# Kernel tuning notes

Measured on AMD Instinct MI355X. Metric: run time of the kernel, lower is better.

The kernel has to match this reference:

```python
import jax, jax.numpy as jnp
import numpy as np

HS = 2048   # hidden_size
NH = 16     # num_attention_heads
HD = HS // NH  # head_dim = 128
FD = 256    # feature_dim
EPS = 1e-5  # layer_norm_epsilon


def setup_inputs() -> dict:
    key = jax.random.key(0)
    ks = jax.random.split(key, 12)
    s = 0.02
    return {
        "hidden_states": jax.random.normal(ks[0], (2, 4096, HS), jnp.float32),
        "attention_mask": jnp.zeros((2, 4096), jnp.float32),
        "Wq": jax.random.normal(ks[1], (HS, HS), jnp.float32) * s,
        "bq": jnp.zeros((HS,), jnp.float32),
        "Wk": jax.random.normal(ks[2], (HS, HS), jnp.float32) * s,
        "bk": jnp.zeros((HS,), jnp.float32),
        "Wv": jax.random.normal(ks[3], (HS, HS), jnp.float32) * s,
        "bv": jnp.zeros((HS,), jnp.float32),
        "Wo": jax.random.normal(ks[4], (HS, HS), jnp.float32) * s,
        "bo": jnp.zeros((HS,), jnp.float32),
        "Wf1": jax.random.normal(ks[5], (HD, FD), jnp.float32) * s,
        "bf1": jnp.zeros((FD,), jnp.float32),
        "Wf2": jax.random.normal(ks[6], (FD, FD), jnp.float32) * s,
        "bf2": jnp.zeros((FD,), jnp.float32),
        "ln_g": jnp.ones((FD,), jnp.float32),
        "ln_b": jnp.zeros((FD,), jnp.float32),
    }


def reference(hidden_states, attention_mask, Wq, bq, Wk, bk, Wv, bv, Wo, bo,
              Wf1, bf1, Wf2, bf2, ln_g, ln_b):
    B, L, H = hidden_states.shape

    # QKV projections -> [B, NH, L, HD]
    q = (hidden_states @ Wq + bq).reshape(B, L, NH, HD).transpose(0, 2, 1, 3)
    k = (hidden_states @ Wk + bk).reshape(B, L, NH, HD).transpose(0, 2, 1, 3)
    v = (hidden_states @ Wv + bv).reshape(B, L, NH, HD).transpose(0, 2, 1, 3)

    # seq_len (4096) > linear_threshold (1024) -> linear attention branch
    def feature_map(x):  # Linear -> ReLU -> Linear -> LayerNorm
        h = jax.nn.relu(x @ Wf1 + bf1)
        h = h @ Wf2 + bf2
        mu = jnp.mean(h, axis=-1, keepdims=True)
        var = jnp.var(h, axis=-1, keepdims=True)  # biased, like torch LayerNorm
        return (h - mu) * jax.lax.rsqrt(var + EPS) * ln_g + ln_b

    q_feat = feature_map(q)  # [B, NH, L, FD]
    k_feat = feature_map(k)
    # attention_mask [B, L] -> k_feat * (1 + mask)
    k_feat = k_feat * (1.0 + attention_mask[:, None, :, None])

    kv = jnp.einsum('bhlf,bhld->bhfd', k_feat, v)          # [B, NH, FD, HD]
    attn = jnp.einsum('bhlf,bhfd->bhld', q_feat, kv)       # [B, NH, L, HD]
    k_sum = jnp.sum(k_feat, axis=2)                         # [B, NH, FD]
    denom = jnp.einsum('bhlf,bhf->bhl', q_feat, k_sum)[..., None]
    attn = attn / (denom + 1e-8)

    attn = attn.transpose(0, 2, 1, 3).reshape(B, L, H)
    return attn @ Wo + bo
```

## Files before the change

kernel.cpp:

```cpp
#include <hip/hip_runtime.h>

typedef unsigned short u16;
typedef unsigned int u32;
typedef __attribute__((ext_vector_type(8))) short bf16x8;
typedef __attribute__((ext_vector_type(4))) float f32x4;

#define B_ 2
#define L_ 4096
#define HS_ 2048
#define NH_ 16
#define HD_ 128
#define FD_ 256

__device__ __forceinline__ float bf2f(u16 u) { return __uint_as_float(((u32)u) << 16); }
__device__ __forceinline__ u16 f2bf(float f) {
    u32 x = __float_as_uint(f);
    return (u16)((x + 0x7fffu + ((x >> 16) & 1u)) >> 16);
}

__device__ __forceinline__ void llds16(const u16* g, u16* l) {
    __builtin_amdgcn_global_load_lds((const __attribute__((address_space(1))) void*)g,
                                     (__attribute__((address_space(3))) void*)l, 16, 0, 0);
}

__device__ __forceinline__ void gemm_mainloop(const u16* __restrict__ Ab, int lda,
                                              const u16* __restrict__ Bb, int ldb,
                                              int K, u16* As, u16* Bs, f32x4 (&acc)[4][4]) {
    const int tid  = threadIdx.x;
    const int lane = tid & 63;
    const int wave = tid >> 6;
    const int wm = wave >> 1, wn = wave & 1;

    f32x4 zero = {0.f, 0.f, 0.f, 0.f};
#pragma unroll
    for (int i = 0; i < 4; i++)
#pragma unroll
        for (int j = 0; j < 4; j++) acc[i][j] = zero;

    const int srow = lane >> 2;
    const int scol = (lane & 3) * 8;
    const u16* pa = Ab + (size_t)(wave * 32 + srow) * lda + scol;
    const u16* pb = Bb + (size_t)(wave * 32 + srow) * ldb + scol;
    u16* la = As + wave * 1024;
    u16* lb = Bs + wave * 1024;

    const int arow = (wm * 64 + (lane & 15)) * 32 + (lane >> 4) * 8;
    const int brow = (wn * 64 + (lane & 15)) * 32 + (lane >> 4) * 8;

    for (int k0 = 0; k0 < K; k0 += 32) {
        llds16(pa, la);
        llds16(pa + 16 * lda, la + 512);
        llds16(pb, lb);
        llds16(pb + 16 * ldb, lb + 512);
        pa += 32; pb += 32;
        __syncthreads();
        bf16x8 af[4], bg[4];
#pragma unroll
        for (int mt = 0; mt < 4; mt++) af[mt] = *(const bf16x8*)(As + arow + mt * 512);
#pragma unroll
        for (int nt = 0; nt < 4; nt++) bg[nt] = *(const bf16x8*)(Bs + brow + nt * 512);
#pragma unroll
        for (int mt = 0; mt < 4; mt++)
#pragma unroll
            for (int nt = 0; nt < 4; nt++)
                acc[mt][nt] = __builtin_amdgcn_mfma_f32_16x16x32_bf16(af[mt], bg[nt], acc[mt][nt], 0, 0, 0);
        __syncthreads();
    }
}

__global__ __launch_bounds__(256) void k_cvt(const float* __restrict__ src, u16* __restrict__ dst) {
    size_t i = ((size_t)blockIdx.x * 256 + threadIdx.x) * 8;
    float4 a = *(const float4*)(src + i);
    float4 b = *(const float4*)(src + i + 4);
    union { u16 h[8]; uint4 v; } o;
    o.h[0] = f2bf(a.x); o.h[1] = f2bf(a.y); o.h[2] = f2bf(a.z); o.h[3] = f2bf(a.w);
    o.h[4] = f2bf(b.x); o.h[5] = f2bf(b.y); o.h[6] = f2bf(b.z); o.h[7] = f2bf(b.w);
    *(uint4*)(dst + i) = o.v;
}

__global__ __launch_bounds__(256) void k_transpose(const float* Wq, const float* Wk, const float* Wv,
                                                   const float* Wo, const float* Wf1, const float* Wf2,
                                                   u16* Wqkv_t, u16* Wo_t, u16* Wf1_t, u16* Wf2_t) {
    const float* src; u16* dst; int R, C;
    switch (blockIdx.z) {
        case 0: src = Wq;  dst = Wqkv_t;                R = 2048; C = 2048; break;
        case 1: src = Wk;  dst = Wqkv_t + 2048 * 2048;  R = 2048; C = 2048; break;
        case 2: src = Wv;  dst = Wqkv_t + 2 * 2048 * 2048; R = 2048; C = 2048; break;
        case 3: src = Wo;  dst = Wo_t;                  R = 2048; C = 2048; break;
        case 4: src = Wf1; dst = Wf1_t;                 R = 128;  C = 256;  break;
        default: src = Wf2; dst = Wf2_t;                R = 256;  C = 256;  break;
    }
    int c0 = blockIdx.x * 32, r0 = blockIdx.y * 32;
    if (c0 >= C || r0 >= R) return;
    __shared__ u16 tile[32][33];
    int tx = threadIdx.x, ty = threadIdx.y;
    for (int i = ty; i < 32; i += 8) tile[i][tx] = f2bf(src[(size_t)(r0 + i) * C + c0 + tx]);
    __syncthreads();
    for (int i = ty; i < 32; i += 8) dst[(size_t)(c0 + i) * R + r0 + tx] = tile[tx][i];
}

#define QKV_BAR() { __builtin_amdgcn_sched_barrier(0); __builtin_amdgcn_s_barrier(); \
                    __builtin_amdgcn_sched_barrier(0); }
#define QKV_LGKM0() { asm volatile("s_waitcnt lgkmcnt(0)" ::: "memory"); \
                      __builtin_amdgcn_sched_barrier(0); }

__device__ __forceinline__ void mainloop256(const u16* __restrict__ Abase,
                                            const u16* __restrict__ Bbase,
                                            u16* LDS, f32x4 (&acc)[8][4]) {
    const int tid = threadIdx.x, lane = tid & 63, wave = tid >> 6;
    const int wm = wave >> 2, wn = wave & 3;

    int r0g, c0g, r1g, c1g;
    { int p = tid * 16; int s = p >> 10, q = p & 1023; q ^= ((q >> 9) & 1) << 5;
      r0g = (s >> 1) * 16 + (q >> 6); c0g = (s & 1) * 32 + ((q & 63) >> 1); }
    { int p = 8192 + tid * 16; int s = p >> 10, q = p & 1023; q ^= ((q >> 9) & 1) << 5;
      r1g = (s >> 1) * 16 + (q >> 6); c1g = (s & 1) * 32 + ((q & 63) >> 1); }
    const int voff0 = r0g * HS_ + c0g;
    const int voff1 = r1g * HS_ + c1g;

    int qby = (lane & 15) * 64 + (lane >> 4) * 16;
    qby ^= ((qby >> 9) & 1) << 5;
    const int qh = qby >> 1;

#define STG(G, soff, dstu) { \
    llds16((G) + (soff) + voff0, LDS + (dstu) + wave * 512); \
    llds16((G) + (soff) + voff1, LDS + (dstu) + 4096 + wave * 512); }

    const size_t a0 = 0, a1 = (size_t)128 * HS_;
    const size_t b0 = 0, b1 = (size_t)128 * HS_;

    STG(Bbase, b0, 32768); STG(Bbase, b1, 40960);
    STG(Abase, a0, 0);     STG(Abase, a1, 8192);
    STG(Bbase, b0 + 64, 49152); STG(Bbase, b1 + 64, 57344);
    STG(Abase, a0 + 64, 16384);
    asm volatile("s_waitcnt vmcnt(6)" ::: "memory");
    QKV_BAR();

    f32x4 zero = {0.f, 0.f, 0.f, 0.f};
#pragma unroll
    for (int i = 0; i < 8; i++)
#pragma unroll
        for (int j = 0; j < 4; j++) acc[i][j] = zero;

    const int NT = HS_ / 64;
    bf16x8 afr[4][2], bfr[4][2];
    for (int t = 0; t < NT; t++) {
        const int bsel = t & 1;
        const u16* Ah = LDS + bsel * 16384 + wm * 8192;
        const u16* Bh = LDS + 32768 + bsel * 16384 + (wn >> 1) * 8192;
        const int bg0 = (wn & 1) * 4;
        const size_t kc1 = (size_t)(t + 1) * 64, kc2 = (size_t)(t + 2) * 64;

#pragma unroll
        for (int mf = 0; mf < 4; mf++)
#pragma unroll
            for (int ks = 0; ks < 2; ks++)
                afr[mf][ks] = *(const bf16x8*)(Ah + (mf * 2 + ks) * 512 + qh);
#pragma unroll
        for (int nf = 0; nf < 4; nf++)
#pragma unroll
            for (int ks = 0; ks < 2; ks++)
                bfr[nf][ks] = *(const bf16x8*)(Bh + ((bg0 + nf) * 2 + ks) * 512 + qh);
        if (t + 1 < NT) STG(Abase, a1 + kc1, (bsel ^ 1) * 16384 + 8192);
        QKV_BAR();
        QKV_LGKM0();
        __builtin_amdgcn_s_setprio(1);
#pragma unroll
        for (int mf = 0; mf < 4; mf++)
#pragma unroll
            for (int nf = 0; nf < 2; nf++)
#pragma unroll
                for (int ks = 0; ks < 2; ks++)
                    acc[mf][nf] = __builtin_amdgcn_mfma_f32_16x16x32_bf16(afr[mf][ks], bfr[nf][ks], acc[mf][nf], 0, 0, 0);
        __builtin_amdgcn_s_setprio(0);
        QKV_BAR();
        if (t + 2 < NT) STG(Bbase, b0 + kc2, 32768 + bsel * 16384);
        QKV_BAR();
        __builtin_amdgcn_s_setprio(1);
#pragma unroll
        for (int mf = 0; mf < 4; mf++)
#pragma unroll
            for (int nf = 2; nf < 4; nf++)
#pragma unroll
                for (int ks = 0; ks < 2; ks++)
                    acc[mf][nf] = __builtin_amdgcn_mfma_f32_16x16x32_bf16(afr[mf][ks], bfr[nf][ks], acc[mf][nf], 0, 0, 0);
        __builtin_amdgcn_s_setprio(0);
        QKV_BAR();
#pragma unroll
        for (int mf = 0; mf < 4; mf++)
#pragma unroll
            for (int ks = 0; ks < 2; ks++)
                afr[mf][ks] = *(const bf16x8*)(Ah + ((mf + 4) * 2 + ks) * 512 + qh);
        if (t + 2 < NT) STG(Bbase, b1 + kc2, 32768 + bsel * 16384 + 8192);
        QKV_BAR();
        QKV_LGKM0();
        __builtin_amdgcn_s_setprio(1);
#pragma unroll
        for (int mf = 0; mf < 4; mf++)
#pragma unroll
            for (int nf = 0; nf < 2; nf++)
#pragma unroll
                for (int ks = 0; ks < 2; ks++)
                    acc[mf + 4][nf] = __builtin_amdgcn_mfma_f32_16x16x32_bf16(afr[mf][ks], bfr[nf][ks], acc[mf + 4][nf], 0, 0, 0);
        __builtin_amdgcn_s_setprio(0);
        QKV_BAR();
        if (t + 2 < NT) STG(Abase, a0 + kc2, bsel * 16384);
        QKV_BAR();
        __builtin_amdgcn_s_setprio(1);
#pragma unroll
        for (int mf = 0; mf < 4; mf++)
#pragma unroll
            for (int nf = 2; nf < 4; nf++)
#pragma unroll
                for (int ks = 0; ks < 2; ks++)
                    acc[mf + 4][nf] = __builtin_amdgcn_mfma_f32_16x16x32_bf16(afr[mf][ks], bfr[nf][ks], acc[mf + 4][nf], 0, 0, 0);
        __builtin_amdgcn_s_setprio(0);
        if (t + 2 < NT) { asm volatile("s_waitcnt vmcnt(6)" ::: "memory"); }
        else if (t + 1 < NT) { asm volatile("s_waitcnt vmcnt(0)" ::: "memory"); }
        QKV_BAR();
    }
#undef STG
}

__global__ __launch_bounds__(512, 2) void k_gemm_qkv(
        const u16* __restrict__ X, const u16* __restrict__ Wt,
        const float* __restrict__ bq, const float* __restrict__ bk, const float* __restrict__ bv,
        u16* __restrict__ qout, u16* __restrict__ kout, u16* __restrict__ vT) {
    __shared__ u16 LDS[65536];
    const int tid = threadIdx.x, lane = tid & 63, wave = tid >> 6;
    const int wm = wave >> 2, wn = wave & 3;

    const int xcd = blockIdx.x & 7, r = blockIdx.x >> 3;
    const int nblk = xcd * 3 + (r >> 5);
    const int mblk = r & 31;
    const int mb = mblk * 256, nb = nblk * 256;

    f32x4 acc[8][4];
    mainloop256(X + (size_t)mb * HS_, Wt + (size_t)nb * HS_, LDS, acc);

    const int which = nblk >> 3;
    const int colbase = (nblk & 7) * 256;
    const int bi = mb >> 12, lb = mb & 4095;
    const float* bias = (which == 0) ? bq : (which == 1 ? bk : bv);
    const int rb = (lane >> 4) << 2, cl = lane & 15;

    if (which < 2) {
        u16* dst = (which == 0) ? qout : kout;
        const int bh0 = bi * NH_ + (colbase >> 7);
        for (int half = 0; half < 2; half++) {
            if (wm == half) {
#pragma unroll
                for (int nf = 0; nf < 4; nf++) {
                    float bvv = bias[colbase + wn * 64 + nf * 16 + cl];
#pragma unroll
                    for (int mf = 0; mf < 8; mf++)
#pragma unroll
                        for (int r2 = 0; r2 < 4; r2++)
                            LDS[(mf * 16 + rb + r2) * 264 + wn * 64 + nf * 16 + cl] =
                                f2bf(acc[mf][nf][r2] + bvv);
                }
            }
            __syncthreads();
#pragma unroll
            for (int it = 0; it < 8; it++) {
                int row = (tid >> 5) + it * 16;
                int c8 = (tid & 31) * 8;
                uint2 lo = *(const uint2*)(LDS + row * 264 + c8);
                uint2 hi = *(const uint2*)(LDS + row * 264 + c8 + 4);
                uint4 val = make_uint4(lo.x, lo.y, hi.x, hi.y);
                u16* pp = dst + ((size_t)(bh0 + (c8 >> 7)) * L_ + lb + half * 128 + row) * HD_ + (c8 & 127);
                *(uint4*)pp = val;
            }
            __syncthreads();
        }
    } else {
        for (int half = 0; half < 2; half++) {
            if (wm == half) {
#pragma unroll
                for (int nf = 0; nf < 4; nf++) {
                    float bvv = bias[colbase + wn * 64 + nf * 16 + cl];
#pragma unroll
                    for (int mf = 0; mf < 8; mf++)
#pragma unroll
                        for (int r2 = 0; r2 < 4; r2++)
                            LDS[(wn * 64 + nf * 16 + cl) * 136 + mf * 16 + rb + r2] =
                                f2bf(acc[mf][nf][r2] + bvv);
                }
            }
            __syncthreads();
#pragma unroll
            for (int it = 0; it < 8; it++) {
                int n = (tid >> 4) + it * 32;
                int c8 = (tid & 15) * 8;
                uint2 lo = *(const uint2*)(LDS + n * 136 + c8);
                uint2 hi = *(const uint2*)(LDS + n * 136 + c8 + 4);
                uint4 val = make_uint4(lo.x, lo.y, hi.x, hi.y);
                int cg = colbase + n;
                u16* pp = vT + ((size_t)(bi * NH_ + (cg >> 7)) * HD_ + (cg & 127)) * L_ + lb + half * 128 + c8;
                *(uint4*)pp = val;
            }
            __syncthreads();
        }
    }
}

__global__ __launch_bounds__(512, 2) void k_gemm_out(const u16* __restrict__ A, const u16* __restrict__ Wt,
                                                     const float* __restrict__ bo, float* __restrict__ out) {
    __shared__ u16 LDS[65536];
    const int lane = threadIdx.x & 63, wave = threadIdx.x >> 6;
    const int wm = wave >> 2, wn = wave & 3;

    const int xcd = blockIdx.x & 7, idx = blockIdx.x >> 3;
    const int nblk = xcd;
    const int mblk = idx;
    const int mb = mblk * 256, nb = nblk * 256;

    f32x4 acc[8][4];
    mainloop256(A + (size_t)mb * HS_, Wt + (size_t)nb * HS_, LDS, acc);

    const int rb = (lane >> 4) << 2, cl = lane & 15;
#pragma unroll
    for (int nf = 0; nf < 4; nf++) {
        int n = nb + wn * 64 + nf * 16 + cl;
        float bvv = bo[n];
#pragma unroll
        for (int mf = 0; mf < 8; mf++) {
            int m = mb + wm * 128 + mf * 16 + rb;
#pragma unroll
            for (int r = 0; r < 4; r++)
                out[(size_t)(m + r) * HS_ + n] = acc[mf][nf][r] + bvv;
        }
    }
}

template <int MASKED, int TRANS>
__global__ __launch_bounds__(256) void k_feat(const u16* __restrict__ X,
                                              const u16* __restrict__ W1t, const float* __restrict__ b1,
                                              const u16* __restrict__ W2t, const float* __restrict__ b2,
                                              const float* __restrict__ g, const float* __restrict__ be,
                                              const float* __restrict__ mask, const float* __restrict__ ksum,
                                              const u16* __restrict__ kvT,
                                              u16* __restrict__ feat, float* __restrict__ ksp,
                                              u16* __restrict__ attnOut) {
    __shared__ u16 As[64 * 32];
    __shared__ u16 Bs[256 * 32];
    __shared__ u16 H[64 * 264];
    __shared__ float MU[64], RS[64], FAC[64], RD[64];
    const int tid = threadIdx.x, lane = tid & 63, wave = tid >> 6;
    const int mb = blockIdx.x * 64;

    const int srow = lane >> 2, scol = (lane & 3) * 8;
    const int arow_rd = (lane & 15);
    const int kgrp = (lane >> 4) * 8;

    f32x4 acc[4][4];
    f32x4 zero = {0.f, 0.f, 0.f, 0.f};
#pragma unroll
    for (int i = 0; i < 4; i++)
#pragma unroll
        for (int j = 0; j < 4; j++) acc[i][j] = zero;

    for (int k0 = 0; k0 < 128; k0 += 32) {
        llds16(X + (size_t)(mb + wave * 16 + srow) * 128 + k0 + scol, As + wave * 512);
#pragma unroll
        for (int i = 0; i < 4; i++)
            llds16(W1t + (size_t)((wave * 4 + i) * 16 + srow) * 128 + k0 + scol,
                   Bs + (wave * 4 + i) * 512);
        __syncthreads();
        bf16x8 af[4], bg[4];
#pragma unroll
        for (int mt = 0; mt < 4; mt++) af[mt] = *(const bf16x8*)(As + (mt * 16 + arow_rd) * 32 + kgrp);
#pragma unroll
        for (int nt = 0; nt < 4; nt++) bg[nt] = *(const bf16x8*)(Bs + (wave * 64 + nt * 16 + arow_rd) * 32 + kgrp);
#pragma unroll
        for (int mt = 0; mt < 4; mt++)
#pragma unroll
            for (int nt = 0; nt < 4; nt++)
                acc[mt][nt] = __builtin_amdgcn_mfma_f32_16x16x32_bf16(af[mt], bg[nt], acc[mt][nt], 0, 0, 0);
        __syncthreads();
    }
    {
        const int rbase = (lane >> 4) << 2;
#pragma unroll
        for (int nt = 0; nt < 4; nt++) {
            int n = wave * 64 + nt * 16 + (lane & 15);
            float bvv = b1[n];
#pragma unroll
            for (int mt = 0; mt < 4; mt++)
#pragma unroll
                for (int r = 0; r < 4; r++) {
                    float v = fmaxf(acc[mt][nt][r] + bvv, 0.f);
                    H[(mt * 16 + rbase + r) * 264 + n] = f2bf(v);
                }
            acc[0][nt] = zero; acc[1][nt] = zero; acc[2][nt] = zero; acc[3][nt] = zero;
        }
    }
    __syncthreads();

    for (int k0 = 0; k0 < 256; k0 += 32) {
#pragma unroll
        for (int i = 0; i < 4; i++)
            llds16(W2t + (size_t)((wave * 4 + i) * 16 + srow) * 256 + k0 + scol,
                   Bs + (wave * 4 + i) * 512);
        __syncthreads();
        bf16x8 af[4], bg[4];
#pragma unroll
        for (int mt = 0; mt < 4; mt++) af[mt] = *(const bf16x8*)(H + (mt * 16 + arow_rd) * 264 + k0 + kgrp);
#pragma unroll
        for (int nt = 0; nt < 4; nt++) bg[nt] = *(const bf16x8*)(Bs + (wave * 64 + nt * 16 + arow_rd) * 32 + kgrp);
#pragma unroll
        for (int mt = 0; mt < 4; mt++)
#pragma unroll
            for (int nt = 0; nt < 4; nt++)
                acc[mt][nt] = __builtin_amdgcn_mfma_f32_16x16x32_bf16(af[mt], bg[nt], acc[mt][nt], 0, 0, 0);
        __syncthreads();
    }
    {
        const int rbase = (lane >> 4) << 2;
#pragma unroll
        for (int nt = 0; nt < 4; nt++) {
            int n = wave * 64 + nt * 16 + (lane & 15);
            float bvv = b2[n];
#pragma unroll
            for (int mt = 0; mt < 4; mt++)
#pragma unroll
                for (int r = 0; r < 4; r++)
                    H[(mt * 16 + rbase + r) * 264 + n] = f2bf(acc[mt][nt][r] + bvv);
        }
    }
    __syncthreads();

    {
        for (int r = 0; r < 16; r++) {
            int row = wave * 16 + r;
            int j = lane * 4;
            uint2 u = *(const uint2*)(H + row * 264 + j);
            float x0 = bf2f((u16)(u.x & 0xffff)), x1 = bf2f((u16)(u.x >> 16));
            float x2 = bf2f((u16)(u.y & 0xffff)), x3 = bf2f((u16)(u.y >> 16));
            float s = x0 + x1 + x2 + x3;
            float ss = x0 * x0 + x1 * x1 + x2 * x2 + x3 * x3;
#pragma unroll
            for (int o = 32; o >= 1; o >>= 1) { s += __shfl_xor(s, o); ss += __shfl_xor(ss, o); }
            if (lane == 0) {
                float mu = s * (1.f / FD_);
                float var = ss * (1.f / FD_) - mu * mu;
                MU[row] = mu;
                RS[row] = rsqrtf(var + 1e-5f);
                float fac = 1.f;
                if (MASKED) {
                    int grow = mb + row;
                    int b = grow >> 16;
                    int l = grow & 4095;
                    fac = 1.f + mask[b * L_ + l];
                }
                FAC[row] = fac;
            }
        }
    }
    __syncthreads();

    if (!TRANS) {
        const int bh = mb >> 12;
        const u16* kvTb = kvT + (size_t)bh * HD_ * FD_;
        {
            int j = lane * 4;
            float4 gg = *(const float4*)(g + j);
            float4 bb = *(const float4*)(be + j);
            float4 kk = *(const float4*)(ksum + (size_t)bh * FD_ + j);
            for (int r = 0; r < 16; r++) {
                int row = wave * 16 + r;
                float mu = MU[row], rstd = RS[row], fac = FAC[row];
                uint2 u = *(const uint2*)(H + row * 264 + j);
                float x0 = bf2f((u16)(u.x & 0xffff)), x1 = bf2f((u16)(u.x >> 16));
                float x2 = bf2f((u16)(u.y & 0xffff)), x3 = bf2f((u16)(u.y >> 16));
                u16 h0 = f2bf(((x0 - mu) * rstd * gg.x + bb.x) * fac);
                u16 h1 = f2bf(((x1 - mu) * rstd * gg.y + bb.y) * fac);
                u16 h2 = f2bf(((x2 - mu) * rstd * gg.z + bb.z) * fac);
                u16 h3 = f2bf(((x3 - mu) * rstd * gg.w + bb.w) * fac);
                uint2 o2;
                o2.x = (u32)h0 | ((u32)h1 << 16);
                o2.y = (u32)h2 | ((u32)h3 << 16);
                *(uint2*)(H + row * 264 + j) = o2;
                float dp = bf2f(h0) * kk.x + bf2f(h1) * kk.y + bf2f(h2) * kk.z + bf2f(h3) * kk.w;
#pragma unroll
                for (int o = 32; o >= 1; o >>= 1) dp += __shfl_xor(dp, o);
                if (lane == 0) RD[row] = 1.f / (dp + 1e-8f);
            }
        }
        __syncthreads();
        f32x4 pacc[8];
#pragma unroll
        for (int i = 0; i < 8; i++) pacc[i] = zero;
        for (int k0 = 0; k0 < 256; k0 += 32) {
            llds16(kvTb + (size_t)(wave * 32 + srow) * FD_ + k0 + scol, Bs + (wave * 32) * 32);
            llds16(kvTb + (size_t)(wave * 32 + 16 + srow) * FD_ + k0 + scol, Bs + (wave * 32 + 16) * 32);
            __syncthreads();
            bf16x8 af = *(const bf16x8*)(H + (wave * 16 + arow_rd) * 264 + k0 + kgrp);
#pragma unroll
            for (int nt = 0; nt < 8; nt++) {
                bf16x8 bg = *(const bf16x8*)(Bs + (nt * 16 + arow_rd) * 32 + kgrp);
                pacc[nt] = __builtin_amdgcn_mfma_f32_16x16x32_bf16(af, bg, pacc[nt], 0, 0, 0);
            }
            __syncthreads();
        }
        const int rbase = (lane >> 4) << 2, cl = lane & 15;
#pragma unroll
        for (int nt = 0; nt < 8; nt++)
#pragma unroll
            for (int r = 0; r < 4; r++) {
                int row = wave * 16 + rbase + r;
                H[row * 264 + nt * 16 + cl] = f2bf(pacc[nt][r] * RD[row]);
            }
        __syncthreads();
        const int b = bh >> 4, h = bh & 15, lb = mb & 4095;
        const int c8 = (tid & 15) * 8;
#pragma unroll
        for (int it = 0; it < 4; it++) {
            int row = (tid >> 4) + it * 16;
            uint2 lo = *(const uint2*)(H + row * 264 + c8);
            uint2 hi = *(const uint2*)(H + row * 264 + c8 + 4);
            *(uint4*)(attnOut + ((size_t)(b * L_ + lb + row)) * HS_ + h * HD_ + c8) =
                make_uint4(lo.x, lo.y, hi.x, hi.y);
        }
    } else {
        int f = tid;
        int bh = mb >> 12, lb = mb & 4095;
        float gf = g[f], bf = be[f];
        u16* orow = feat + ((size_t)bh * FD_ + f) * L_ + lb;
        float fsum = 0.f;
        for (int lg = 0; lg < 64; lg += 8) {
            union { u16 h8[8]; uint4 v4; } pk;
#pragma unroll
            for (int j = 0; j < 8; j++) {
                int row = lg + j;
                float x = bf2f(H[row * 264 + f]);
                float y = ((x - MU[row]) * RS[row] * gf + bf) * FAC[row];
                fsum += y;
                pk.h8[j] = f2bf(y);
            }
            *(uint4*)(orow + lg) = pk.v4;
        }
        ksp[((size_t)bh * 64 + (lb >> 6)) * FD_ + f] = fsum;
    }
}

__global__ __launch_bounds__(256) void k_ksum2(const float* __restrict__ ksp, float* __restrict__ ksum) {
    const int bh = blockIdx.x, f = threadIdx.x;
    float s = 0.f;
    for (int i = 0; i < 64; i++) s += ksp[((size_t)bh * 64 + i) * FD_ + f];
    ksum[(size_t)bh * FD_ + f] = s;
}

__global__ __launch_bounds__(256) void k_gemm_kv(const u16* __restrict__ kfT, const u16* __restrict__ vT,
                                                 float* __restrict__ kvp) {
    __shared__ u16 As[4096], Bs[4096];
    f32x4 acc[4][4];
    const int mb = blockIdx.x * 128;
    const int ks = blockIdx.y;
    const int bh = blockIdx.z;
    gemm_mainloop(kfT + ((size_t)bh * FD_ + mb) * L_ + ks * 1024, L_,
                  vT + (size_t)bh * HD_ * L_ + ks * 1024, L_, 1024, As, Bs, acc);
    const int lane = threadIdx.x & 63, wave = threadIdx.x >> 6;
    const int wm = wave >> 1, wn = wave & 1;
    const int n0 = wn * 64 + (lane & 15);
    const int m0 = mb + wm * 64 + ((lane >> 4) << 2);
    float* o = kvp + (size_t)(ks * 32 + bh) * (FD_ * HD_);
#pragma unroll
    for (int nt = 0; nt < 4; nt++)
#pragma unroll
        for (int mt = 0; mt < 4; mt++)
#pragma unroll
            for (int r = 0; r < 4; r++)
                o[(size_t)(m0 + mt * 16 + r) * HD_ + n0 + nt * 16] = acc[mt][nt][r];
}

__global__ __launch_bounds__(256) void k_kvred(const float* __restrict__ kvp, u16* __restrict__ kvT) {
    const int p = blockIdx.x, bh = blockIdx.y, t = threadIdx.x;
    const int e0 = p * 4096 + t * 16;
    float s[16];
#pragma unroll
    for (int i = 0; i < 16; i++) s[i] = 0.f;
    for (int c = 0; c < 4; c++) {
        const float* src = kvp + ((size_t)(c * 32 + bh)) * 32768 + e0;
#pragma unroll
        for (int i = 0; i < 16; i += 4) {
            float4 vv = *(const float4*)(src + i);
            s[i] += vv.x; s[i + 1] += vv.y; s[i + 2] += vv.z; s[i + 3] += vv.w;
        }
    }
#pragma unroll
    for (int i = 0; i < 16; i++) {
        int e = e0 + i, fq = e >> 7, d = e & 127;
        kvT[((size_t)bh * HD_ + d) * FD_ + fq] = f2bf(s[i]);
    }
}

extern "C" void kernel_launch(void* const* d_in, const int* in_sizes, int n_in,
                              void* d_out, int out_size, void* d_ws, size_t ws_size,
                              hipStream_t stream) {
    const float* hs  = (const float*)d_in[0];
    const float* msk = (const float*)d_in[1];
    const float* Wq  = (const float*)d_in[2];  const float* bq  = (const float*)d_in[3];
    const float* Wk  = (const float*)d_in[4];  const float* bk  = (const float*)d_in[5];
    const float* Wv  = (const float*)d_in[6];  const float* bv  = (const float*)d_in[7];
    const float* Wo  = (const float*)d_in[8];  const float* bo  = (const float*)d_in[9];
    const float* Wf1 = (const float*)d_in[10]; const float* bf1 = (const float*)d_in[11];
    const float* Wf2 = (const float*)d_in[12]; const float* bf2 = (const float*)d_in[13];
    const float* lng = (const float*)d_in[14]; const float* lnb = (const float*)d_in[15];
    float* out = (float*)d_out;
    char* w = (char*)d_ws;

    u16* Wqkv_t = (u16*)(w + 0);
    u16* Xbf    = (u16*)(w + 25165824u);
    u16* kfT    = (u16*)(w + 67108864u);
    u16* qbuf   = (u16*)(w + 134217728u);
    u16* kbuf   = (u16*)(w + 167772160u);
    float* kvp  = (float*)(w + 167772160u);
    u16* attn   = (u16*)(w + 167772160u);
    u16* vT     = (u16*)(w + 201326592u);
    u16* Wo_t   = (u16*)(w + 234881024u);
    u16* Wf1_t  = (u16*)(w + 243269632u);
    u16* Wf2_t  = (u16*)(w + 243335168u);
    float* ksp  = (float*)(w + 243466240u);
    u16* kvT    = (u16*)(w + 245563392u);
    float* ksum = (float*)(w + 247660544u);

    k_cvt<<<dim3(8192), 256, 0, stream>>>(hs, Xbf);
    k_transpose<<<dim3(64, 64, 6), dim3(32, 8), 0, stream>>>(Wq, Wk, Wv, Wo, Wf1, Wf2,
                                                             Wqkv_t, Wo_t, Wf1_t, Wf2_t);
    k_gemm_qkv<<<dim3(768), 512, 0, stream>>>(Xbf, Wqkv_t, bq, bk, bv, qbuf, kbuf, vT);
    k_feat<1, 1><<<dim3(2048), 256, 0, stream>>>(kbuf, Wf1_t, bf1, Wf2_t, bf2, lng, lnb, msk,
                                                 nullptr, nullptr, kfT, ksp, nullptr);
    k_ksum2<<<dim3(32), 256, 0, stream>>>(ksp, ksum);
    k_gemm_kv<<<dim3(2, 4, 32), 256, 0, stream>>>(kfT, vT, kvp);
    k_kvred<<<dim3(8, 32), 256, 0, stream>>>(kvp, kvT);
    k_feat<0, 0><<<dim3(2048), 256, 0, stream>>>(qbuf, Wf1_t, bf1, Wf2_t, bf2, lng, lnb, msk,
                                                 ksum, kvT, nullptr, nullptr, attn);
    k_gemm_out<<<dim3(256), 512, 0, stream>>>(attn, Wo_t, bo, out);
}
```

Measured before the change: 671.3 us.

## Remap QKV GEMM block-to-XCD assignment and double K-step in feature kernel

The QKV GEMM changes how block indices map to M/N tiles. Each XCD now owns a group of M row-blocks and iterates across N tiles, which should improve L2 reuse of the activation rows within an XCD. The feature-map kernel's three MFMA loops now load 64-wide K slices per iteration instead of 32, with LDS buffers enlarged to match. This halves the number of barrier pairs and global-to-LDS rounds, at the cost of more LDS and register use.

Measured after the change: 657.5 us. 2.1% less time.

```diff
diff --git a/kernel.cpp b/kernel.cpp
--- a/kernel.cpp
+++ b/kernel.cpp
@@ -230,9 +230,9 @@
     const int tid = threadIdx.x, lane = tid & 63, wave = tid >> 6;
     const int wm = wave >> 2, wn = wave & 3;
 
-    const int xcd = blockIdx.x & 7, r = blockIdx.x >> 3;
-    const int nblk = xcd * 3 + (r >> 5);
-    const int mblk = r & 31;
+    const int xcd = blockIdx.x & 7, idx = blockIdx.x >> 3;
+    const int nblk = idx >> 2;
+    const int mblk = xcd * 4 + (idx & 3);
     const int mb = mblk * 256, nb = nblk * 256;
 
     f32x4 acc[8][4];
@@ -342,8 +342,8 @@
                                               const u16* __restrict__ kvT,
                                               u16* __restrict__ feat, float* __restrict__ ksp,
                                               u16* __restrict__ attnOut) {
-    __shared__ u16 As[64 * 32];
-    __shared__ u16 Bs[256 * 32];
+    __shared__ u16 As[2 * 2048];
+    __shared__ u16 Bs[2 * 8192];
     __shared__ u16 H[64 * 264];
     __shared__ float MU[64], RS[64], FAC[64], RD[64];
     const int tid = threadIdx.x, lane = tid & 63, wave = tid >> 6;
@@ -360,23 +360,36 @@
 #pragma unroll
         for (int j = 0; j < 4; j++) acc[i][j] = zero;
 
-    for (int k0 = 0; k0 < 128; k0 += 32) {
-        llds16(X + (size_t)(mb + wave * 16 + srow) * 128 + k0 + scol, As + wave * 512);
-#pragma unroll
-        for (int i = 0; i < 4; i++)
-            llds16(W1t + (size_t)((wave * 4 + i) * 16 + srow) * 128 + k0 + scol,
-                   Bs + (wave * 4 + i) * 512);
-        __syncthreads();
-        bf16x8 af[4], bg[4];
-#pragma unroll
-        for (int mt = 0; mt < 4; mt++) af[mt] = *(const bf16x8*)(As + (mt * 16 + arow_rd) * 32 + kgrp);
-#pragma unroll
-        for (int nt = 0; nt < 4; nt++) bg[nt] = *(const bf16x8*)(Bs + (wave * 64 + nt * 16 + arow_rd) * 32 + kgrp);
+    for (int k0 = 0; k0 < 128; k0 += 64) {
+#pragma unroll
+        for (int ks = 0; ks < 2; ks++)
+            llds16(X + (size_t)(mb + wave * 16 + srow) * 128 + k0 + ks * 32 + scol,
+                   As + ks * 2048 + wave * 512);
+#pragma unroll
+        for (int i = 0; i < 8; i++) {
+            int ks = i & 1, rg = i >> 1;
+            llds16(W1t + (size_t)(wave * 64 + rg * 16 + srow) * 128 + k0 + ks * 32 + scol,
+                   Bs + ks * 8192 + wave * 2048 + rg * 512);
+        }
+        __syncthreads();
+        bf16x8 af[4][2], bg[4][2];
 #pragma unroll
         for (int mt = 0; mt < 4; mt++)
 #pragma unroll
+            for (int ks = 0; ks < 2; ks++)
+                af[mt][ks] = *(const bf16x8*)(As + ks * 2048 + (mt * 16 + arow_rd) * 32 + kgrp);
+#pragma unroll
+        for (int nt = 0; nt < 4; nt++)
+#pragma unroll
+            for (int ks = 0; ks < 2; ks++)
+                bg[nt][ks] = *(const bf16x8*)(Bs + ks * 8192 + (wave * 64 + nt * 16 + arow_rd) * 32 + kgrp);
+#pragma unroll
+        for (int mt = 0; mt < 4; mt++)
+#pragma unroll
             for (int nt = 0; nt < 4; nt++)
-                acc[mt][nt] = __builtin_amdgcn_mfma_f32_16x16x32_bf16(af[mt], bg[nt], acc[mt][nt], 0, 0, 0);
+#pragma unroll
+                for (int ks = 0; ks < 2; ks++)
+                    acc[mt][nt] = __builtin_amdgcn_mfma_f32_16x16x32_bf16(af[mt][ks], bg[nt][ks], acc[mt][nt], 0, 0, 0);
         __syncthreads();
     }
     {
@@ -397,22 +410,32 @@
     }
     __syncthreads();
 
-    for (int k0 = 0; k0 < 256; k0 += 32) {
-#pragma unroll
-        for (int i = 0; i < 4; i++)
-            llds16(W2t + (size_t)((wave * 4 + i) * 16 + srow) * 256 + k0 + scol,
-                   Bs + (wave * 4 + i) * 512);
-        __syncthreads();
-        bf16x8 af[4], bg[4];
-#pragma unroll
-        for (int mt = 0; mt < 4; mt++) af[mt] = *(const bf16x8*)(H + (mt * 16 + arow_rd) * 264 + k0 + kgrp);
-#pragma unroll
-        for (int nt = 0; nt < 4; nt++) bg[nt] = *(const bf16x8*)(Bs + (wave * 64 + nt * 16 + arow_rd) * 32 + kgrp);
+    for (int k0 = 0; k0 < 256; k0 += 64) {
+#pragma unroll
+        for (int i = 0; i < 8; i++) {
+            int ks = i & 1, rg = i >> 1;
+            llds16(W2t + (size_t)(wave * 64 + rg * 16 + srow) * 256 + k0 + ks * 32 + scol,
+                   Bs + ks * 8192 + wave * 2048 + rg * 512);
+        }
+        __syncthreads();
+        bf16x8 af[4][2], bg[4][2];
 #pragma unroll
         for (int mt = 0; mt < 4; mt++)
 #pragma unroll
+            for (int ks = 0; ks < 2; ks++)
+                af[mt][ks] = *(const bf16x8*)(H + (mt * 16 + arow_rd) * 264 + k0 + ks * 32 + kgrp);
+#pragma unroll
+        for (int nt = 0; nt < 4; nt++)
+#pragma unroll
+            for (int ks = 0; ks < 2; ks++)
+                bg[nt][ks] = *(const bf16x8*)(Bs + ks * 8192 + (wave * 64 + nt * 16 + arow_rd) * 32 + kgrp);
+#pragma unroll
+        for (int mt = 0; mt < 4; mt++)
+#pragma unroll
             for (int nt = 0; nt < 4; nt++)
-                acc[mt][nt] = __builtin_amdgcn_mfma_f32_16x16x32_bf16(af[mt], bg[nt], acc[mt][nt], 0, 0, 0);
+#pragma unroll
+                for (int ks = 0; ks < 2; ks++)
+                    acc[mt][nt] = __builtin_amdgcn_mfma_f32_16x16x32_bf16(af[mt][ks], bg[nt][ks], acc[mt][nt], 0, 0, 0);
         __syncthreads();
     }
     {
@@ -491,16 +514,25 @@
         f32x4 pacc[8];
 #pragma unroll
         for (int i = 0; i < 8; i++) pacc[i] = zero;
-        for (int k0 = 0; k0 < 256; k0 += 32) {
-            llds16(kvTb + (size_t)(wave * 32 + srow) * FD_ + k0 + scol, Bs + (wave * 32) * 32);
-            llds16(kvTb + (size_t)(wave * 32 + 16 + srow) * FD_ + k0 + scol, Bs + (wave * 32 + 16) * 32);
+        for (int k0 = 0; k0 < 256; k0 += 64) {
+#pragma unroll
+            for (int i = 0; i < 4; i++) {
+                int ks = i & 1, rg = i >> 1;
+                llds16(kvTb + (size_t)(wave * 32 + rg * 16 + srow) * 256 + k0 + ks * 32 + scol,
+                       Bs + ks * 4096 + wave * 1024 + rg * 512);
+            }
             __syncthreads();
-            bf16x8 af = *(const bf16x8*)(H + (wave * 16 + arow_rd) * 264 + k0 + kgrp);
-#pragma unroll
-            for (int nt = 0; nt < 8; nt++) {
-                bf16x8 bg = *(const bf16x8*)(Bs + (nt * 16 + arow_rd) * 32 + kgrp);
-                pacc[nt] = __builtin_amdgcn_mfma_f32_16x16x32_bf16(af, bg, pacc[nt], 0, 0, 0);
-            }
+            bf16x8 af[2];
+#pragma unroll
+            for (int ks = 0; ks < 2; ks++)
+                af[ks] = *(const bf16x8*)(H + (wave * 16 + arow_rd) * 264 + k0 + ks * 32 + kgrp);
+#pragma unroll
+            for (int nt = 0; nt < 8; nt++)
+#pragma unroll
+                for (int ks = 0; ks < 2; ks++) {
+                    bf16x8 bg = *(const bf16x8*)(Bs + ks * 4096 + (nt * 16 + arow_rd) * 32 + kgrp);
+                    pacc[nt] = __builtin_amdgcn_mfma_f32_16x16x32_bf16(af[ks], bg, pacc[nt], 0, 0, 0);
+                }
             __syncthreads();
         }
         const int rbase = (lane >> 4) << 2, cl = lane & 15;
```
